# Kernel tuning notes

Hardware: AMD Instinct MI355X
Metric: run time of the kernel (lower is better)

The kernel has to match this reference:

```python
import jax, jax.numpy as jnp
import numpy as np

N_NODES = 10000
N_GRAPHS = 64
NEG_SLOPE = 0.2
EPS = 1e-16


def gat_conv(x, src, dst, W, a_src, a_dst, bias, heads, out_ch, num_nodes):
    """PyG GATConv (shared lin, add_self_loops already applied to src/dst)."""
    xl = (x @ W).reshape(num_nodes, heads, out_ch)          # [N,H,C]
    alpha_s = jnp.einsum('nhc,hc->nh', xl, a_src)           # [N,H]
    alpha_d = jnp.einsum('nhc,hc->nh', xl, a_dst)           # [N,H]
    e = jax.nn.leaky_relu(alpha_s[src] + alpha_d[dst], NEG_SLOPE)  # [E,H]
    # segment softmax over incoming edges of each destination node
    emax = jax.ops.segment_max(e, dst, num_segments=num_nodes)
    emax = jnp.where(jnp.isfinite(emax), emax, 0.0)
    ee = jnp.exp(e - emax[dst])
    denom = jax.ops.segment_sum(ee, dst, num_segments=num_nodes)
    alpha = ee / (denom[dst] + EPS)                         # [E,H]
    msg = xl[src] * alpha[:, :, None]                       # [E,H,C]
    out = jax.ops.segment_sum(msg, dst, num_segments=num_nodes)  # [N,H,C]
    return out.reshape(num_nodes, heads * out_ch) + bias


def setup_inputs() -> dict:
    key = jax.random.key(0)
    ks = jax.random.split(key, 16)
    H, C, IN = 8, 128, 128
    x = jax.random.normal(ks[0], (N_NODES, IN), jnp.float32)
    edge_index = jax.random.randint(ks[1], (2, 320000), 0, N_NODES, jnp.int64)
    batch = jnp.sort(jax.random.randint(ks[2], (N_NODES,), 0, N_GRAPHS, jnp.int64))
    g = lambda k, shp, fan: jax.random.normal(k, shp, jnp.float32) * (1.0 / np.sqrt(fan))
    return {
        'x': x, 'edge_index': edge_index, 'batch': batch,
        'W1': g(ks[3], (IN, H * C), IN),
        'a_src1': g(ks[4], (H, C), C), 'a_dst1': g(ks[5], (H, C), C),
        'b1': jnp.zeros((H * C,), jnp.float32),
        'W2': g(ks[6], (H * C, C), H * C),
        'a_src2': g(ks[7], (1, C), C), 'a_dst2': g(ks[8], (1, C), C),
        'b2': jnp.zeros((C,), jnp.float32),
        'lin1_w': g(ks[9], (C, 128), C), 'lin1_b': jnp.zeros((128,), jnp.float32),
        'lin2_w': g(ks[10], (128, 1), 128), 'lin2_b': jnp.zeros((1,), jnp.float32),
    }


def reference(x, edge_index, batch, W1, a_src1, a_dst1, b1, W2, a_src2, a_dst2, b2,
              lin1_w, lin1_b, lin2_w, lin2_b):
    loops = jnp.arange(N_NODES, dtype=edge_index.dtype)
    src = jnp.concatenate([edge_index[0], loops])
    dst = jnp.concatenate([edge_index[1], loops])
    h = jax.nn.elu(gat_conv(x, src, dst, W1, a_src1, a_dst1, b1, 8, 128, N_NODES))
    h = jax.nn.elu(gat_conv(h, src, dst, W2, a_src2, a_dst2, b2, 1, 128, N_NODES))
    # global mean pool over graphs
    sums = jax.ops.segment_sum(h, batch, num_segments=N_GRAPHS)
    cnts = jax.ops.segment_sum(jnp.ones((N_NODES,), h.dtype), batch, num_segments=N_GRAPHS)
    pooled = sums / jnp.maximum(cnts, 1.0)[:, None]         # [G,128]
    z = jax.nn.relu(pooled @ lin1_w + lin1_b)
    return (z @ lin2_w + lin2_b).squeeze(1)                 # [G]
```

## Files before the change

kernel.cpp:

```cpp
#include <hip/hip_runtime.h>
#include <math.h>

#define N_NODES 10000
#define N_GRAPHS 64
#define E_RAW 320000
#define E_ALL (E_RAW + N_NODES)
#define NEG_SLOPE 0.2f
#define EPS 1e-16f
#define CAP 192

typedef unsigned short ushort_t;
typedef short short8 __attribute__((ext_vector_type(8)));
typedef float floatx4 __attribute__((ext_vector_type(4)));

static __device__ __forceinline__ float bfl(unsigned u) {
  union { unsigned u; float f; } v; v.u = u << 16; return v.f;
}
static __device__ __forceinline__ float bfh(unsigned u) {
  union { unsigned u; float f; } v; v.u = u & 0xFFFF0000u; return v.f;
}
static __device__ __forceinline__ ushort_t f2bf(float f) {
  union { float f; unsigned u; } v; v.f = f;
  unsigned r = v.u + 0x7FFFu + ((v.u >> 16) & 1u);
  return (ushort_t)(r >> 16);
}

static __device__ __forceinline__ void load16_lds(const ushort_t* gp, ushort_t* ldsbase, int lane) {
#if __has_builtin(__builtin_amdgcn_global_load_lds)
  __builtin_amdgcn_global_load_lds((const __attribute__((address_space(1))) void*)gp,
                                   (__attribute__((address_space(3))) void*)ldsbase, 16, 0, 0);
#else
  *(uint4*)(ldsbase + lane * 8) = *(const uint4*)gp;
#endif
}

static __device__ __forceinline__ void swz_one(const float* __restrict__ W,
                                               ushort_t* __restrict__ Wsw,
                                               int idx, int K, int N) {
  int NT = N >> 4;
  int lane = idx & 63, tile = idx >> 6;
  int nt = tile % NT, kt = tile / NT;
  int n = nt * 16 + (lane & 15);
  int kb = kt * 32 + (lane >> 4) * 8;
  ushort4 lo, hi;
  lo.x = f2bf(W[(size_t)(kb + 0) * N + n]); lo.y = f2bf(W[(size_t)(kb + 1) * N + n]);
  lo.z = f2bf(W[(size_t)(kb + 2) * N + n]); lo.w = f2bf(W[(size_t)(kb + 3) * N + n]);
  hi.x = f2bf(W[(size_t)(kb + 4) * N + n]); hi.y = f2bf(W[(size_t)(kb + 5) * N + n]);
  hi.z = f2bf(W[(size_t)(kb + 6) * N + n]); hi.w = f2bf(W[(size_t)(kb + 7) * N + n]);
  *(ushort4*)(Wsw + (size_t)idx * 8) = lo;
  *(ushort4*)(Wsw + (size_t)idx * 8 + 4) = hi;
}

__global__ __launch_bounds__(1024) void prep_k(const float* __restrict__ x,
                                               const int* __restrict__ batch,
                                               const float* __restrict__ W1,
                                               const float* __restrict__ W2,
                                               ushort_t* __restrict__ xb,
                                               ushort_t* __restrict__ W1sw,
                                               ushort_t* __restrict__ W2sw,
                                               float* __restrict__ zero0,
                                               int* __restrict__ poolcnt) {
  __shared__ int shm[N_GRAPHS];
  const int b = blockIdx.x, t = threadIdx.x;
  if (b < 49) {
    int i4 = b * 1024 + t;
    if (i4 < 49548) *(float4*)(zero0 + i4 * 4) = make_float4(0.f, 0.f, 0.f, 0.f);
  } else if (b == 49) {
    if (t < N_GRAPHS) shm[t] = 0;
    __syncthreads();
    for (int n = t; n < N_NODES; n += 1024) atomicAdd(&shm[batch[n]], 1);
    __syncthreads();
    if (t < N_GRAPHS) poolcnt[t] = shm[t];
  } else if (b < 363) {
    int i4 = (b - 50) * 1024 + t;
    if (i4 < 320000) {
      float4 v = *(const float4*)(x + (size_t)i4 * 4);
      ushort4 o;
      o.x = f2bf(v.x); o.y = f2bf(v.y); o.z = f2bf(v.z); o.w = f2bf(v.w);
      *(ushort4*)(xb + (size_t)i4 * 4) = o;
    }
  } else if (b < 379) {
    int idx = (b - 363) * 1024 + t;
    if (idx < 16384) swz_one(W1, W1sw, idx, 128, 1024);
  } else {
    int idx = (b - 379) * 1024 + t;
    if (idx < 16384) swz_one(W2, W2sw, idx, 1024, 128);
  }
}

__global__ __launch_bounds__(256) void g1f_k(const ushort_t* __restrict__ A,
                                             const ushort_t* __restrict__ Bsw,
                                             ushort_t* __restrict__ Cb,
                                             const float* __restrict__ aS,
                                             const float* __restrict__ aD,
                                             float* __restrict__ asO,
                                             float* __restrict__ adO,
                                             const int* __restrict__ ei,
                                             int* __restrict__ degc,
                                             int* __restrict__ csr) {
  __shared__ ushort_t Albuf[32 * 512];
  __shared__ float epi[4][16][68];
  const int bid = blockIdx.x, t = threadIdx.x;
  if (bid >= 632) {
    int e = (bid - 632) * 256 + t;
    if (e < E_ALL) {
      int s, d;
      if (e < E_RAW) { s = ei[e]; d = ei[E_RAW + e]; }
      else           { s = d = e - E_RAW; }
      int pos = atomicAdd(&degc[d], 1);
      if (pos < CAP) csr[d * CAP + pos] = s;
    }
    return;
  }
  const int M = N_NODES, K = 128, NT = 64;
  const int lane = t & 63, w = t >> 6;
  const int wm = w >> 1, wn = w & 1;
  const int m0 = (bid >> 3) * 128;
  const int n0 = (bid & 7) * 128;
  const int g = lane >> 4, l16 = lane & 15;

  #pragma unroll
  for (int i = 0; i < 8; i++) {
    int tile = w * 8 + i;
    int mtl = tile >> 2, kt = tile & 3;
    int r = m0 + mtl * 16 + l16; r = r < M ? r : M - 1;
    load16_lds(A + (size_t)r * K + kt * 32 + g * 8, &Albuf[tile * 512], lane);
  }
  __syncthreads();

  floatx4 acc[4][4] = {};
  #pragma unroll
  for (int kt = 0; kt < 4; kt++) {
    short8 a[4], b[4];
    #pragma unroll
    for (int mi = 0; mi < 4; mi++)
      a[mi] = *(const short8*)&Albuf[(((wm * 4 + mi) * 4 + kt) * 64 + lane) * 8];
    #pragma unroll
    for (int ni = 0; ni < 4; ni++) {
      int nt = (n0 >> 4) + wn * 4 + ni;
      b[ni] = *(const short8*)(Bsw + ((size_t)(kt * NT + nt) * 64 + lane) * 8);
    }
    #pragma unroll
    for (int mi = 0; mi < 4; mi++)
      #pragma unroll
      for (int ni = 0; ni < 4; ni++)
        acc[mi][ni] = __builtin_amdgcn_mfma_f32_16x16x32_bf16(a[mi], b[ni], acc[mi][ni], 0, 0, 0);
  }

  const int h = bid & 7;
  const int r = lane >> 2, c0 = (lane & 3) * 16;
  const int colh = wn * 64 + c0;
  float asc[16], adc[16];
  #pragma unroll
  for (int c = 0; c < 16; c++) { asc[c] = aS[h * 128 + colh + c]; adc[c] = aD[h * 128 + colh + c]; }
  #pragma unroll
  for (int mi = 0; mi < 4; mi++) {
    #pragma unroll
    for (int ni = 0; ni < 4; ni++)
      #pragma unroll
      for (int reg = 0; reg < 4; reg++)
        epi[w][g * 4 + reg][ni * 16 + l16] = acc[mi][ni][reg];
    float4 v0 = *(float4*)&epi[w][r][c0];
    float4 v1 = *(float4*)&epi[w][r][c0 + 4];
    float4 v2 = *(float4*)&epi[w][r][c0 + 8];
    float4 v3 = *(float4*)&epi[w][r][c0 + 12];
    float vr[16] = {v0.x,v0.y,v0.z,v0.w, v1.x,v1.y,v1.z,v1.w,
                    v2.x,v2.y,v2.z,v2.w, v3.x,v3.y,v3.z,v3.w};
    int grow = m0 + wm * 64 + mi * 16 + r;
    float sp = 0.f, dp = 0.f;
    ushort_t hv[16];
    #pragma unroll
    for (int c = 0; c < 16; c++) {
      sp = fmaf(vr[c], asc[c], sp);
      dp = fmaf(vr[c], adc[c], dp);
      hv[c] = f2bf(vr[c]);
    }
    sp += __shfl_xor(sp, 1); sp += __shfl_xor(sp, 2);
    dp += __shfl_xor(dp, 1); dp += __shfl_xor(dp, 2);
    if (grow < M) {
      uint4 u0, u1;
      u0.x = (unsigned)hv[0] | ((unsigned)hv[1] << 16);
      u0.y = (unsigned)hv[2] | ((unsigned)hv[3] << 16);
      u0.z = (unsigned)hv[4] | ((unsigned)hv[5] << 16);
      u0.w = (unsigned)hv[6] | ((unsigned)hv[7] << 16);
      u1.x = (unsigned)hv[8] | ((unsigned)hv[9] << 16);
      u1.y = (unsigned)hv[10] | ((unsigned)hv[11] << 16);
      u1.z = (unsigned)hv[12] | ((unsigned)hv[13] << 16);
      u1.w = (unsigned)hv[14] | ((unsigned)hv[15] << 16);
      ushort_t* cp = Cb + (size_t)grow * 1024 + (bid & 7) * 128 + wn * 64 + c0;
      *(uint4*)cp = u0;
      *(uint4*)(cp + 8) = u1;
      if ((lane & 3) == 0) {
        atomicAdd(&asO[grow * 8 + h], sp);
        atomicAdd(&adO[grow * 8 + h], dp);
      }
    }
  }
}

__global__ __launch_bounds__(256) void gemm2_k(const ushort_t* __restrict__ A,
                                               const ushort_t* __restrict__ Bsw,
                                               ushort_t* __restrict__ Cb,
                                               const float* __restrict__ aS,
                                               const float* __restrict__ aD,
                                               float* __restrict__ asO,
                                               float* __restrict__ adO) {
  const int M = N_NODES, K = 1024, NT = 8;
  __shared__ ushort_t Albuf[8 * 512];
  __shared__ float epi[4][16][68];
  const int t = threadIdx.x, lane = t & 63, w = t >> 6;
  const int wm = w >> 1, wn = w & 1;
  const int mb0 = blockIdx.x * 32;
  const int g = lane >> 4, l16 = lane & 15;

  floatx4 acc[4] = {};
  for (int ch = 0; ch < 8; ch++) {
    #pragma unroll
    for (int i = 0; i < 2; i++) {
      int tile = w * 2 + i;
      int mtl = tile >> 2, kt = tile & 3;
      int r = mb0 + mtl * 16 + l16; r = r < M ? r : M - 1;
      load16_lds(A + (size_t)r * K + (ch * 4 + kt) * 32 + g * 8, &Albuf[tile * 512], lane);
    }
    __syncthreads();
    #pragma unroll
    for (int ks = 0; ks < 4; ks++) {
      short8 a = *(const short8*)&Albuf[(((wm * 4 + ks)) * 64 + lane) * 8];
      #pragma unroll
      for (int ni = 0; ni < 4; ni++) {
        int nt = wn * 4 + ni, ktg = ch * 4 + ks;
        short8 b = *(const short8*)(Bsw + ((size_t)(ktg * NT + nt) * 64 + lane) * 8);
        acc[ni] = __builtin_amdgcn_mfma_f32_16x16x32_bf16(a, b, acc[ni], 0, 0, 0);
      }
    }
    __syncthreads();
  }

  const int r = lane >> 2, c0 = (lane & 3) * 16;
  const int colh = wn * 64 + c0;
  float asc[16], adc[16];
  #pragma unroll
  for (int c = 0; c < 16; c++) { asc[c] = aS[colh + c]; adc[c] = aD[colh + c]; }
  #pragma unroll
  for (int ni = 0; ni < 4; ni++)
    #pragma unroll
    for (int reg = 0; reg < 4; reg++)
      epi[w][g * 4 + reg][ni * 16 + l16] = acc[ni][reg];
  float4 v0 = *(float4*)&epi[w][r][c0];
  float4 v1 = *(float4*)&epi[w][r][c0 + 4];
  float4 v2 = *(float4*)&epi[w][r][c0 + 8];
  float4 v3 = *(float4*)&epi[w][r][c0 + 12];
  float vr[16] = {v0.x,v0.y,v0.z,v0.w, v1.x,v1.y,v1.z,v1.w,
                  v2.x,v2.y,v2.z,v2.w, v3.x,v3.y,v3.z,v3.w};
  int grow = mb0 + wm * 16 + r;
  float sp = 0.f, dp = 0.f;
  ushort_t hv[16];
  #pragma unroll
  for (int c = 0; c < 16; c++) {
    sp = fmaf(vr[c], asc[c], sp);
    dp = fmaf(vr[c], adc[c], dp);
    hv[c] = f2bf(vr[c]);
  }
  sp += __shfl_xor(sp, 1); sp += __shfl_xor(sp, 2);
  dp += __shfl_xor(dp, 1); dp += __shfl_xor(dp, 2);
  if (grow < M) {
    uint4 u0, u1;
    u0.x = (unsigned)hv[0] | ((unsigned)hv[1] << 16);
    u0.y = (unsigned)hv[2] | ((unsigned)hv[3] << 16);
    u0.z = (unsigned)hv[4] | ((unsigned)hv[5] << 16);
    u0.w = (unsigned)hv[6] | ((unsigned)hv[7] << 16);
    u1.x = (unsigned)hv[8] | ((unsigned)hv[9] << 16);
    u1.y = (unsigned)hv[10] | ((unsigned)hv[11] << 16);
    u1.z = (unsigned)hv[12] | ((unsigned)hv[13] << 16);
    u1.w = (unsigned)hv[14] | ((unsigned)hv[15] << 16);
    ushort_t* cp = Cb + (size_t)grow * 128 + colh;
    *(uint4*)cp = u0;
    *(uint4*)(cp + 8) = u1;
    if ((lane & 3) == 0) {
      atomicAdd(&asO[grow], sp);
      atomicAdd(&adO[grow], dp);
    }
  }
}

__global__ __launch_bounds__(64) void agg1_k(const ushort_t* __restrict__ xlb,
                                             const float* __restrict__ as1,
                                             const float* __restrict__ ad1,
                                             const float* __restrict__ b1,
                                             const int* __restrict__ degc,
                                             const int* __restrict__ csr,
                                             ushort_t* __restrict__ out) {
  const int bid = blockIdx.x, t = threadIdx.x;
  const int h = bid & 7, dst = bid >> 3;
  int deg = degc[dst]; deg = deg < CAP ? deg : CAP;
  const int beg = dst * CAP;
  const int degp = (deg + 7) & ~7;
  __shared__ uint2 pr[CAP];
  float adh = ad1[dst * 8 + h];
  if (deg <= 64) {
    bool act = t < deg;
    int s = act ? csr[beg + t] : 0;
    float lg = -1e30f;
    if (act) {
      float v = as1[s * 8 + h] + adh;
      lg = v > 0.f ? v : NEG_SLOPE * v;
    }
    float pm = lg;
    #pragma unroll
    for (int off = 32; off; off >>= 1) pm = fmaxf(pm, __shfl_xor(pm, off));
    float ex = act ? __expf(lg - pm) : 0.f;
    float ps = ex;
    #pragma unroll
    for (int off = 32; off; off >>= 1) ps += __shfl_xor(ps, off);
    float inv = 1.0f / (ps + EPS);
    if (t < degp) pr[t] = act ? make_uint2((unsigned)(s * 2048), __float_as_uint(ex * inv))
                              : make_uint2(0u, 0u);
    __syncthreads();
  } else {
    __shared__ int ssg[CAP];
    __shared__ float alg[CAP];
    for (int e = t; e < deg; e += 64) ssg[e] = csr[beg + e];
    __syncthreads();
    float pm = -1e30f;
    for (int e = t; e < deg; e += 64) {
      float v = as1[ssg[e] * 8 + h] + adh;
      v = v > 0.f ? v : NEG_SLOPE * v;
      alg[e] = v;
      pm = fmaxf(pm, v);
    }
    #pragma unroll
    for (int off = 32; off; off >>= 1) pm = fmaxf(pm, __shfl_xor(pm, off));
    __syncthreads();
    float ps = 0.f;
    for (int e = t; e < deg; e += 64) ps += __expf(alg[e] - pm);
    #pragma unroll
    for (int off = 32; off; off >>= 1) ps += __shfl_xor(ps, off);
    float inv = 1.0f / (ps + EPS);
    for (int e = t; e < deg; e += 64)
      pr[e] = make_uint2((unsigned)(ssg[e] * 2048), __float_as_uint(__expf(alg[e] - pm) * inv));
    for (int e = deg + t; e < degp; e += 64) pr[e] = make_uint2(0u, 0u);
    __syncthreads();
  }
  const char* xbase = (const char*)xlb;
  const unsigned toff = (unsigned)(h * 256 + 4 * t);
  float accA[4] = {}, accB[4] = {};
  for (int e0 = 0; e0 < degp; e0 += 8) {
    #pragma unroll
    for (int j = 0; j < 8; j++) {
      uint2 p = pr[e0 + j];
      unsigned u = *(const unsigned*)(xbase + (p.x + toff));
      float a = __uint_as_float(p.y);
      accA[j & 3] = fmaf(a, bfl(u), accA[j & 3]);
      accB[j & 3] = fmaf(a, bfh(u), accB[j & 3]);
    }
  }
  float acc0 = (accA[0] + accA[1]) + (accA[2] + accA[3]);
  float acc1 = (accB[0] + accB[1]) + (accB[2] + accB[3]);
  int o = h * 128 + 2 * t;
  float v0 = acc0 + b1[o];
  float v1 = acc1 + b1[o + 1];
  v0 = v0 > 0.f ? v0 : (__expf(v0) - 1.0f);
  v1 = v1 > 0.f ? v1 : (__expf(v1) - 1.0f);
  unsigned up = (unsigned)f2bf(v0) | ((unsigned)f2bf(v1) << 16);
  *(unsigned*)(out + (size_t)dst * 1024 + o) = up;
}

__global__ __launch_bounds__(64) void agg2_k(const ushort_t* __restrict__ xlb2,
                                             const float* __restrict__ as2,
                                             const float* __restrict__ ad2,
                                             const float* __restrict__ b2,
                                             const int* __restrict__ degc,
                                             const int* __restrict__ csr,
                                             const int* __restrict__ batch,
                                             float* __restrict__ poolsum) {
  int dst = blockIdx.x, t = threadIdx.x;
  int deg = degc[dst]; deg = deg < CAP ? deg : CAP;
  int beg = dst * CAP;
  const int degp = (deg + 7) & ~7;
  float adv = ad2[dst];
  __shared__ uint2 pr[CAP];
  if (deg <= 64) {
    bool act = t < deg;
    int s = act ? csr[beg + t] : 0;
    float lg = -1e30f;
    if (act) {
      float v = as2[s] + adv;
      lg = v > 0.f ? v : NEG_SLOPE * v;
    }
    float pm = lg;
    #pragma unroll
    for (int off = 32; off; off >>= 1) pm = fmaxf(pm, __shfl_xor(pm, off));
    float ex = act ? __expf(lg - pm) : 0.f;
    float ps = ex;
    #pragma unroll
    for (int off = 32; off; off >>= 1) ps += __shfl_xor(ps, off);
    float inv = 1.0f / (ps + EPS);
    if (t < degp) pr[t] = act ? make_uint2((unsigned)(s * 256), __float_as_uint(ex * inv))
                              : make_uint2(0u, 0u);
    __syncthreads();
  } else {
    __shared__ int ssg[CAP];
    __shared__ float alg[CAP];
    for (int e = t; e < deg; e += 64) ssg[e] = csr[beg + e];
    __syncthreads();
    float pm = -1e30f;
    for (int e = t; e < deg; e += 64) {
      float v = as2[ssg[e]] + adv;
      v = v > 0.f ? v : NEG_SLOPE * v;
      alg[e] = v;
      pm = fmaxf(pm, v);
    }
    #pragma unroll
    for (int off = 32; off; off >>= 1) pm = fmaxf(pm, __shfl_xor(pm, off));
    __syncthreads();
    float ps = 0.f;
    for (int e = t; e < deg; e += 64) ps += __expf(alg[e] - pm);
    #pragma unroll
    for (int off = 32; off; off >>= 1) ps += __shfl_xor(ps, off);
    float inv = 1.0f / (ps + EPS);
    for (int e = t; e < deg; e += 64)
      pr[e] = make_uint2((unsigned)(ssg[e] * 256), __float_as_uint(__expf(alg[e] - pm) * inv));
    for (int e = deg + t; e < degp; e += 64) pr[e] = make_uint2(0u, 0u);
    __syncthreads();
  }
  const char* xbase = (const char*)xlb2;
  const unsigned toff = (unsigned)(4 * t);
  float accA[4] = {}, accB[4] = {};
  for (int e0 = 0; e0 < degp; e0 += 8) {
    #pragma unroll
    for (int j = 0; j < 8; j++) {
      uint2 p = pr[e0 + j];
      unsigned u = *(const unsigned*)(xbase + (p.x + toff));
      float a = __uint_as_float(p.y);
      accA[j & 3] = fmaf(a, bfl(u), accA[j & 3]);
      accB[j & 3] = fmaf(a, bfh(u), accB[j & 3]);
    }
  }
  float acc0 = (accA[0] + accA[1]) + (accA[2] + accA[3]);
  float acc1 = (accB[0] + accB[1]) + (accB[2] + accB[3]);
  int c0 = 2 * t;
  float v0 = acc0 + b2[c0];
  float v1 = acc1 + b2[c0 + 1];
  v0 = v0 > 0.f ? v0 : (__expf(v0) - 1.0f);
  v1 = v1 > 0.f ? v1 : (__expf(v1) - 1.0f);
  int g = batch[dst];
  atomicAdd(&poolsum[g * 128 + c0], v0);
  atomicAdd(&poolsum[g * 128 + c0 + 1], v1);
}

__global__ __launch_bounds__(128) void final_k(const float* __restrict__ poolsum,
                                               const int* __restrict__ cnt,
                                               const float* __restrict__ l1w,
                                               const float* __restrict__ l1b,
                                               const float* __restrict__ l2w,
                                               const float* __restrict__ l2b,
                                               float* __restrict__ out) {
  int g = blockIdx.x, t = threadIdx.x;
  __shared__ float pooled[128];
  float c = fmaxf((float)cnt[g], 1.0f);
  pooled[t] = poolsum[g * 128 + t] / c;
  __syncthreads();
  float acc = l1b[t];
  for (int i = 0; i < 128; i++) acc = fmaf(pooled[i], l1w[i * 128 + t], acc);
  acc = fmaxf(acc, 0.0f);
  float p = acc * l2w[t];
  #pragma unroll
  for (int off = 32; off; off >>= 1) p += __shfl_down(p, off);
  __shared__ float r[2];
  if ((t & 63) == 0) r[t >> 6] = p;
  __syncthreads();
  if (t == 0) out[g] = r[0] + r[1] + l2b[0];
}

extern "C" void kernel_launch(void* const* d_in, const int* in_sizes, int n_in,
                              void* d_out, int out_size, void* d_ws, size_t ws_size,
                              hipStream_t stream) {
  const float* x    = (const float*)d_in[0];
  const int*   ei   = (const int*)d_in[1];
  const int*   batch= (const int*)d_in[2];
  const float* W1   = (const float*)d_in[3];
  const float* aS1  = (const float*)d_in[4];
  const float* aD1  = (const float*)d_in[5];
  const float* b1   = (const float*)d_in[6];
  const float* W2   = (const float*)d_in[7];
  const float* aS2  = (const float*)d_in[8];
  const float* aD2  = (const float*)d_in[9];
  const float* b2   = (const float*)d_in[10];
  const float* l1w  = (const float*)d_in[11];
  const float* l1b  = (const float*)d_in[12];
  const float* l2w  = (const float*)d_in[13];
  const float* l2b  = (const float*)d_in[14];
  float* out = (float*)d_out;

  ushort_t* xlb1   = (ushort_t*)d_ws;
  ushort_t* h1b    = xlb1 + 10240000;
  ushort_t* xlb2   = h1b + 10240000;
  ushort_t* xb     = xlb2 + 1280000;
  ushort_t* W1sw   = xb + 1280000;
  ushort_t* W2sw   = W1sw + 131072;
  float*    zero0  = (float*)(W2sw + 131072);
  float*    as1    = zero0;
  float*    ad1    = as1 + 80000;
  float*    as2    = ad1 + 80000;
  float*    ad2    = as2 + 10000;
  float*    poolsum= ad2 + 10000;
  int*      degc   = (int*)(poolsum + 8192);
  int*      poolcnt= degc + 10000;
  int*      csr    = poolcnt + 64;

  prep_k<<<395, 1024, 0, stream>>>(x, batch, W1, W2, xb, W1sw, W2sw, zero0, poolcnt);
  g1f_k<<<632 + 1290, 256, 0, stream>>>(xb, W1sw, xlb1, aS1, aD1, as1, ad1, ei, degc, csr);
  agg1_k<<<N_NODES * 8, 64, 0, stream>>>(xlb1, as1, ad1, b1, degc, csr, h1b);
  gemm2_k<<<313, 256, 0, stream>>>(h1b, W2sw, xlb2, aS2, aD2, as2, ad2);
  agg2_k<<<N_NODES, 64, 0, stream>>>(xlb2, as2, ad2, b2, degc, csr, batch, poolsum);
  final_k<<<N_GRAPHS, 128, 0, stream>>>(poolsum, poolcnt, l1w, l1b, l2w, l2b, out);
}
```

Before: 214.6 us.

## Gather 16-byte feature chunks per lane in GAT aggregation with shuffle reduction

Both aggregation kernels used to have each lane load 4 bytes (2 bf16 channels) for each of the 8 edges in a group. Now 16 lanes cover one 256-byte row with 16-byte loads, and the four lane groups each take different edges, two per iteration. The partial sums are combined across lane groups with a butterfly of xor-shuffles (offsets 32 and 16), and the output channel mapping is changed to match. The aim is fewer, wider memory instructions in the gather; the cost is more accumulator registers and extra shuffle and select work in the epilogue.

```diff
diff --git a/kernel.cpp b/kernel.cpp
--- a/kernel.cpp
+++ b/kernel.cpp
@@ -341,24 +341,49 @@
     for (int e = deg + t; e < degp; e += 64) pr[e] = make_uint2(0u, 0u);
     __syncthreads();
   }
-  const char* xbase = (const char*)xlb;
-  const unsigned toff = (unsigned)(h * 256 + 4 * t);
-  float accA[4] = {}, accB[4] = {};
+  const int g = t >> 4, sub = t & 15;
+  const char* xbase = (const char*)xlb + (h * 256 + 16 * sub);
+  float acc[8] = {};
   for (int e0 = 0; e0 < degp; e0 += 8) {
-    #pragma unroll
-    for (int j = 0; j < 8; j++) {
-      uint2 p = pr[e0 + j];
-      unsigned u = *(const unsigned*)(xbase + (p.x + toff));
-      float a = __uint_as_float(p.y);
-      accA[j & 3] = fmaf(a, bfl(u), accA[j & 3]);
-      accB[j & 3] = fmaf(a, bfh(u), accB[j & 3]);
-    }
-  }
-  float acc0 = (accA[0] + accA[1]) + (accA[2] + accA[3]);
-  float acc1 = (accB[0] + accB[1]) + (accB[2] + accB[3]);
-  int o = h * 128 + 2 * t;
-  float v0 = acc0 + b1[o];
-  float v1 = acc1 + b1[o + 1];
+    uint2 pA = pr[e0 + g];
+    uint2 pB = pr[e0 + 4 + g];
+    uint4 qA = *(const uint4*)(xbase + pA.x);
+    uint4 qB = *(const uint4*)(xbase + pB.x);
+    float aA = __uint_as_float(pA.y), aB = __uint_as_float(pB.y);
+    acc[0] = fmaf(aA, bfl(qA.x), acc[0]); acc[1] = fmaf(aA, bfh(qA.x), acc[1]);
+    acc[2] = fmaf(aA, bfl(qA.y), acc[2]); acc[3] = fmaf(aA, bfh(qA.y), acc[3]);
+    acc[4] = fmaf(aA, bfl(qA.z), acc[4]); acc[5] = fmaf(aA, bfh(qA.z), acc[5]);
+    acc[6] = fmaf(aA, bfl(qA.w), acc[6]); acc[7] = fmaf(aA, bfh(qA.w), acc[7]);
+    acc[0] = fmaf(aB, bfl(qB.x), acc[0]); acc[1] = fmaf(aB, bfh(qB.x), acc[1]);
+    acc[2] = fmaf(aB, bfl(qB.y), acc[2]); acc[3] = fmaf(aB, bfh(qB.y), acc[3]);
+    acc[4] = fmaf(aB, bfl(qB.z), acc[4]); acc[5] = fmaf(aB, bfh(qB.z), acc[5]);
+    acc[6] = fmaf(aB, bfl(qB.w), acc[6]); acc[7] = fmaf(aB, bfh(qB.w), acc[7]);
+  }
+  const bool hi32 = (t & 32) != 0;
+  float s0, s1, s2, s3;
+  {
+    float m0 = hi32 ? acc[4] : acc[0], o0 = hi32 ? acc[0] : acc[4];
+    float m1 = hi32 ? acc[5] : acc[1], o1 = hi32 ? acc[1] : acc[5];
+    float m2 = hi32 ? acc[6] : acc[2], o2 = hi32 ? acc[2] : acc[6];
+    float m3 = hi32 ? acc[7] : acc[3], o3 = hi32 ? acc[3] : acc[7];
+    s0 = m0 + __shfl_xor(o0, 32);
+    s1 = m1 + __shfl_xor(o1, 32);
+    s2 = m2 + __shfl_xor(o2, 32);
+    s3 = m3 + __shfl_xor(o3, 32);
+  }
+  const bool hi16 = (t & 16) != 0;
+  float r0, r1;
+  {
+    float m0 = hi16 ? s2 : s0, o0 = hi16 ? s0 : s2;
+    float m1 = hi16 ? s3 : s1, o1 = hi16 ? s1 : s3;
+    r0 = m0 + __shfl_xor(o0, 16);
+    r1 = m1 + __shfl_xor(o1, 16);
+  }
+  const int c = 8 * sub + 2 * g;
+  const int o = h * 128 + c;
+  float2 bb = *(const float2*)(b1 + o);
+  float v0 = r0 + bb.x;
+  float v1 = r1 + bb.y;
   v0 = v0 > 0.f ? v0 : (__expf(v0) - 1.0f);
   v1 = v1 > 0.f ? v1 : (__expf(v1) - 1.0f);
   unsigned up = (unsigned)f2bf(v0) | ((unsigned)f2bf(v1) << 16);
@@ -423,29 +448,53 @@
     for (int e = deg + t; e < degp; e += 64) pr[e] = make_uint2(0u, 0u);
     __syncthreads();
   }
-  const char* xbase = (const char*)xlb2;
-  const unsigned toff = (unsigned)(4 * t);
-  float accA[4] = {}, accB[4] = {};
+  const int g = t >> 4, sub = t & 15;
+  const char* xbase = (const char*)xlb2 + 16 * sub;
+  float acc[8] = {};
   for (int e0 = 0; e0 < degp; e0 += 8) {
-    #pragma unroll
-    for (int j = 0; j < 8; j++) {
-      uint2 p = pr[e0 + j];
-      unsigned u = *(const unsigned*)(xbase + (p.x + toff));
-      float a = __uint_as_float(p.y);
-      accA[j & 3] = fmaf(a, bfl(u), accA[j & 3]);
-      accB[j & 3] = fmaf(a, bfh(u), accB[j & 3]);
-    }
-  }
-  float acc0 = (accA[0] + accA[1]) + (accA[2] + accA[3]);
-  float acc1 = (accB[0] + accB[1]) + (accB[2] + accB[3]);
-  int c0 = 2 * t;
-  float v0 = acc0 + b2[c0];
-  float v1 = acc1 + b2[c0 + 1];
+    uint2 pA = pr[e0 + g];
+    uint2 pB = pr[e0 + 4 + g];
+    uint4 qA = *(const uint4*)(xbase + pA.x);
+    uint4 qB = *(const uint4*)(xbase + pB.x);
+    float aA = __uint_as_float(pA.y), aB = __uint_as_float(pB.y);
+    acc[0] = fmaf(aA, bfl(qA.x), acc[0]); acc[1] = fmaf(aA, bfh(qA.x), acc[1]);
+    acc[2] = fmaf(aA, bfl(qA.y), acc[2]); acc[3] = fmaf(aA, bfh(qA.y), acc[3]);
+    acc[4] = fmaf(aA, bfl(qA.z), acc[4]); acc[5] = fmaf(aA, bfh(qA.z), acc[5]);
+    acc[6] = fmaf(aA, bfl(qA.w), acc[6]); acc[7] = fmaf(aA, bfh(qA.w), acc[7]);
+    acc[0] = fmaf(aB, bfl(qB.x), acc[0]); acc[1] = fmaf(aB, bfh(qB.x), acc[1]);
+    acc[2] = fmaf(aB, bfl(qB.y), acc[2]); acc[3] = fmaf(aB, bfh(qB.y), acc[3]);
+    acc[4] = fmaf(aB, bfl(qB.z), acc[4]); acc[5] = fmaf(aB, bfh(qB.z), acc[5]);
+    acc[6] = fmaf(aB, bfl(qB.w), acc[6]); acc[7] = fmaf(aB, bfh(qB.w), acc[7]);
+  }
+  const bool hi32 = (t & 32) != 0;
+  float s0, s1, s2, s3;
+  {
+    float m0 = hi32 ? acc[4] : acc[0], o0 = hi32 ? acc[0] : acc[4];
+    float m1 = hi32 ? acc[5] : acc[1], o1 = hi32 ? acc[1] : acc[5];
+    float m2 = hi32 ? acc[6] : acc[2], o2 = hi32 ? acc[2] : acc[6];
+    float m3 = hi32 ? acc[7] : acc[3], o3 = hi32 ? acc[3] : acc[7];
+    s0 = m0 + __shfl_xor(o0, 32);
+    s1 = m1 + __shfl_xor(o1, 32);
+    s2 = m2 + __shfl_xor(o2, 32);
+    s3 = m3 + __shfl_xor(o3, 32);
+  }
+  const bool hi16 = (t & 16) != 0;
+  float r0, r1;
+  {
+    float m0 = hi16 ? s2 : s0, o0 = hi16 ? s0 : s2;
+    float m1 = hi16 ? s3 : s1, o1 = hi16 ? s1 : s3;
+    r0 = m0 + __shfl_xor(o0, 16);
+    r1 = m1 + __shfl_xor(o1, 16);
+  }
+  const int c0 = 8 * sub + 2 * g;
+  float2 bb = *(const float2*)(b2 + c0);
+  float v0 = r0 + bb.x;
+  float v1 = r1 + bb.y;
   v0 = v0 > 0.f ? v0 : (__expf(v0) - 1.0f);
   v1 = v1 > 0.f ? v1 : (__expf(v1) - 1.0f);
-  int g = batch[dst];
-  atomicAdd(&poolsum[g * 128 + c0], v0);
-  atomicAdd(&poolsum[g * 128 + c0 + 1], v1);
+  int gb = batch[dst];
+  atomicAdd(&poolsum[gb * 128 + c0], v0);
+  atomicAdd(&poolsum[gb * 128 + c0 + 1], v1);
 }
 
 __global__ __launch_bounds__(128) void final_k(const float* __restrict__ poolsum,
```

Measured after the change: 216.4 us. No clear change (+0.8%).
